# Performance work log

Hardware: AMD Instinct MI355X
Metric: run time of the kernel (lower is better)

The kernel has to match this reference:

```python
import jax, jax.numpy as jnp
import numpy as np
from jax import lax

B, H, W, M, D, HEADS = 4, 32, 32, 16, 128, 4
N = H * W * M
EPS = 1e-5  # torch LayerNorm default


def layer_norm(x, g, b):
    mu = jnp.mean(x, axis=-1, keepdims=True)
    var = jnp.var(x, axis=-1, keepdims=True)
    return (x - mu) * lax.rsqrt(var + EPS) * g + b


def setup_inputs() -> dict:
    key = jax.random.key(0)
    ks = jax.random.split(key, 8)
    s = 0.02  # weight init scale
    return {
        "x1": jax.random.normal(ks[0], (B, N, D), jnp.float32),
        "x2": jax.random.normal(ks[1], (B, N, D), jnp.float32),
        "ln1_g": jnp.ones((D,), jnp.float32),
        "ln1_b": jnp.zeros((D,), jnp.float32),
        "rep_w": jax.random.normal(ks[2], (2 * D, D), jnp.float32) * s,
        "rep_b": jnp.zeros((2 * D,), jnp.float32),
        "aln_g": jnp.ones((2 * D,), jnp.float32),
        "aln_b": jnp.zeros((2 * D,), jnp.float32),
        "ln2_g": jnp.ones((2 * D,), jnp.float32),
        "ln2_b": jnp.zeros((2 * D,), jnp.float32),
        "fc1_w": jax.random.normal(ks[3], (2 * D, 4 * D), jnp.float32) * s,
        "fc1_b": jnp.zeros((4 * D,), jnp.float32),
        "dw_w": jax.random.normal(ks[4], (4 * D, 1, 3, 3, 3), jnp.float32) * s,
        "dw_b": jnp.zeros((4 * D,), jnp.float32),
        "mln_g": jnp.ones((4 * D,), jnp.float32),
        "mln_b": jnp.zeros((4 * D,), jnp.float32),
        "fc2_w": jax.random.normal(ks[5], (4 * D, 2 * D), jnp.float32) * s,
        "fc2_b": jnp.zeros((2 * D,), jnp.float32),
    }


def reference(x1, x2, ln1_g, ln1_b, rep_w, rep_b, aln_g, aln_b, ln2_g, ln2_b,
              fc1_w, fc1_b, dw_w, dw_b, mln_g, mln_b, fc2_w, fc2_b):
    hk = D // HEADS  # head key channels (== head value channels here)

    # shared norm1 applied to both streams
    n1 = layer_norm(x1, ln1_g, ln1_b)
    n2 = layer_norm(x2, ln1_g, ln1_b)

    # linear (softmax-KV) cross attention: K,Q from n2, V from n1
    kq = jnp.transpose(n2, (0, 2, 1)).reshape(B, HEADS, hk, N)
    v = jnp.transpose(n1, (0, 2, 1)).reshape(B, HEADS, hk, N)
    key = jax.nn.softmax(kq, axis=3)    # softmax over tokens N
    query = jax.nn.softmax(kq, axis=2)  # softmax over head channels
    # context: [B,h,hk,hv]; attended: [B,h,hv,N]
    context = jnp.einsum('bhkn,bhvn->bhkv', key, v)
    att = jnp.einsum('bhkv,bhkn->bhvn', context, query)
    agg = att.reshape(B, D, H, W, M)

    # 1x1x1 Conv3d reprojection D -> 2D, then LayerNorm over channels
    rep = jnp.einsum('ed,bdhwm->behwm', rep_w, agg) + rep_b[None, :, None, None, None]
    rep = jnp.transpose(rep.reshape(B, 2 * D, N), (0, 2, 1))
    attn_out = layer_norm(rep, aln_g, aln_b)

    tx = jnp.concatenate([x1, x2], axis=2) + attn_out  # [B,N,2D]

    # MixFFN_skip on norm2(tx)
    y = layer_norm(tx, ln2_g, ln2_b)
    h1 = y @ fc1_w + fc1_b  # [B,N,4D]
    xv = jnp.transpose(h1, (0, 2, 1)).reshape(B, 4 * D, H, W, M)
    dw = lax.conv_general_dilated(
        xv, dw_w, window_strides=(1, 1, 1), padding='SAME',
        dimension_numbers=('NCDHW', 'OIDHW', 'NCDHW'),
        feature_group_count=4 * D) + dw_b[None, :, None, None, None]
    dw = jnp.transpose(dw.reshape(B, 4 * D, N), (0, 2, 1))
    ax = jax.nn.gelu(layer_norm(dw + h1, mln_g, mln_b), approximate=False)
    out = ax @ fc2_w + fc2_b  # [B,N,2D]

    return tx + out
```

## Files before the change

kernel.cpp:

```cpp
#include <hip/hip_runtime.h>
#include <hip/hip_bf16.h>
#include <math.h>

namespace {

typedef __hip_bfloat16 bf16;
typedef __attribute__((ext_vector_type(8))) short bf16x8;
typedef __attribute__((ext_vector_type(4))) float f32x4;

constexpr int B = 4;
constexpr int N = 16384;
constexpr int D = 128;
constexpr int D2 = 256;
constexpr int D4 = 512;
constexpr int HEADS = 4;
constexpr float EPS = 1e-5f;
constexpr long long BN = (long long)B * N;

__device__ __forceinline__ float tof(bf16 x) { return __bfloat162float(x); }
__device__ __forceinline__ bf16 tob(float x) { return __float2bfloat16(x); }
__device__ __forceinline__ float bflo(unsigned u) { union { unsigned i; float f; } c; c.i = u << 16; return c.f; }
__device__ __forceinline__ float bfhi(unsigned u) { union { unsigned i; float f; } c; c.i = u & 0xffff0000u; return c.f; }
__device__ __forceinline__ unsigned short us(float x) {
  union { bf16 h; unsigned short u; } c; c.h = tob(x); return c.u;
}

__device__ __forceinline__ float ldx(const void* p, long long i, int fl) {
  return fl ? ((const float*)p)[i] : tof(((const bf16*)p)[i]);
}
__device__ __forceinline__ void stx(void* p, long long i, int fl, float v) {
  if (fl) ((float*)p)[i] = v; else ((bf16*)p)[i] = tob(v);
}

constexpr size_t OFF_FLAG = 0;
constexpr size_t OFF_KST  = 1024;
constexpr size_t OFF_CTX  = 2048;
constexpr size_t OFF_REPT = 18432;
constexpr size_t OFF_DWW  = 51200;
constexpr size_t OFF_VEC  = 65024;
constexpr size_t OFF_W1S  = 68864;
constexpr size_t OFF_W2S  = 150784;
constexpr size_t OFF_ST1  = 224512;
constexpr size_t OFF_ST2  = 355584;
constexpr size_t OFF_ST3  = 486656;
constexpr size_t OFF_H1   = 617728;

constexpr int CCH = 128;
constexpr size_t OFF_PARTC = OFF_H1;
constexpr size_t OFF_PARTK = OFF_H1 + 2162688;
constexpr size_t OFF_MREP = OFF_H1;

constexpr int V_LN1G = 0, V_LN1B = 128, V_REPB = 256, V_ALNG = 512, V_ALNB = 768,
              V_LN2G = 1024, V_LN2B = 1280, V_FC1B = 1536, V_DWB = 2048,
              V_MLNG = 2560, V_MLNB = 3072, V_FC2B = 3584;

__global__ void k_detect(const unsigned* __restrict__ g1raw, int* __restrict__ flag) {
  if (threadIdx.x == 0 && blockIdx.x == 0)
    *flag = (g1raw[0] == 0x3F800000u) ? 1 : 0;
}

constexpr int CVT_TOTAL = 32768 + 13824 + 3840 + 163840 + 147456;
__global__ __launch_bounds__(256) void k_cvt(const void* rep_w, const void* fc1_w,
                                             const void* fc2_w, const void* dw_w,
                                             const void* ln1_g, const void* ln1_b,
                                             const void* rep_b, const void* aln_g,
                                             const void* aln_b, const void* ln2_g,
                                             const void* ln2_b, const void* fc1_b,
                                             const void* dw_b, const void* mln_g,
                                             const void* mln_b, const void* fc2_b,
                                             float* __restrict__ ws,
                                             const int* __restrict__ flag) {
  int i = blockIdx.x * 256 + threadIdx.x;
  if (i >= CVT_TOTAL) return;
  int fl = *flag;
  if (i < 32768) {
    int e = i >> 7, d = i & 127;
    ws[OFF_REPT + d * D2 + e] = ldx(rep_w, i, fl);
  } else if (i < 46592) {
    int j = i - 32768; ws[OFF_DWW + j] = ldx(dw_w, j, fl);
  } else if (i < 50432) {
    int j = i - 46592;
    const void* src; int off;
    if      (j < 128)  { src = ln1_g; off = j - V_LN1G; }
    else if (j < 256)  { src = ln1_b; off = j - V_LN1B; }
    else if (j < 512)  { src = rep_b; off = j - V_REPB; }
    else if (j < 768)  { src = aln_g; off = j - V_ALNG; }
    else if (j < 1024) { src = aln_b; off = j - V_ALNB; }
    else if (j < 1280) { src = ln2_g; off = j - V_LN2G; }
    else if (j < 1536) { src = ln2_b; off = j - V_LN2B; }
    else if (j < 2048) { src = fc1_b; off = j - V_FC1B; }
    else if (j < 2560) { src = dw_b;  off = j - V_DWB; }
    else if (j < 3072) { src = mln_g; off = j - V_MLNG; }
    else if (j < 3584) { src = mln_b; off = j - V_MLNB; }
    else               { src = fc2_b; off = j - V_FC2B; }
    ws[OFF_VEC + j] = ldx(src, off, fl);
  } else if (i < 214272) {
    int j = i - 50432;
    int kc = j / 20480, rem = j % 20480;
    int n = rem / 40, kk = rem % 40;
    float v = (kk < 32) ? ldx(fc1_w, (kc * 32 + kk) * 512 + n, fl) : 0.f;
    ((unsigned short*)(ws + OFF_W1S))[j] = us(v);
  } else {
    int j = i - 214272;
    int kc = j / 18432, rem = j % 18432;
    int n = rem / 72, kk = rem % 72;
    float v = (kk < 64) ? ldx(fc2_w, (kc * 64 + kk) * 256 + n, fl) : 0.f;
    ((unsigned short*)(ws + OFF_W2S))[j] = us(v);
  }
}

__global__ __launch_bounds__(256) void k_rowstats(const void* __restrict__ x1,
                                                  const void* __restrict__ x2,
                                                  float2* __restrict__ st1,
                                                  float2* __restrict__ st2,
                                                  const int* __restrict__ flag) {
  int fl = *flag;
  int wid = threadIdx.x >> 6;
  int lane = threadIdx.x & 63;
  long long row = (long long)blockIdx.x * 4 + wid;
  const void* src;
  float2* dst;
  long long r;
  if (row < BN) { src = x1; dst = st1; r = row; }
  else          { src = x2; dst = st2; r = row - BN; }
  float a = ldx(src, r * D + lane, fl);
  float b = ldx(src, r * D + lane + 64, fl);
  float s = a + b, ss = a * a + b * b;
  for (int off = 32; off; off >>= 1) {
    s  += __shfl_xor(s, off, 64);
    ss += __shfl_xor(ss, off, 64);
  }
  if (lane == 0) {
    float mu = s * (1.0f / D);
    float var = fmaxf(ss * (1.0f / D) - mu * mu, 0.f);
    dst[r] = make_float2(mu, rsqrtf(var + EPS));
  }
}

__global__ __launch_bounds__(256) void k_kstats_part(const void* __restrict__ x2,
                                                     const float2* __restrict__ st2,
                                                     const float* __restrict__ vec,
                                                     float2* __restrict__ part,
                                                     const int* __restrict__ flag) {
  __shared__ float2 st[256];
  __shared__ float sm[128], ssum[128];
  int fl = *flag;
  int t = threadIdx.x;
  int bc = blockIdx.x;
  int b = bc >> 6;
  int chunk = bc & 63;
  long long tokbase = (long long)b * N + chunk * 256;
  st[t] = st2[tokbase + t];
  __syncthreads();
  int g = t >> 7, c = t & 127;
  float gc = vec[V_LN1G + c], bcv = vec[V_LN1B + c];
  float m = -INFINITY, s = 0.f;
  for (int i = 0; i < 128; i++) {
    int nl = g * 128 + i;
    float2 a2 = st[nl];
    float x = (ldx(x2, (tokbase + nl) * D + c, fl) - a2.x) * a2.y * gc + bcv;
    if (x > m) { s = s * expf(m - x) + 1.f; m = x; }
    else       { s += expf(x - m); }
  }
  if (g == 1) { sm[c] = m; ssum[c] = s; }
  __syncthreads();
  if (g == 0) {
    float m2 = sm[c], s2 = ssum[c];
    float M = fmaxf(m, m2);
    float S = s * expf(m - M) + s2 * expf(m2 - M);
    part[bc * 128 + c] = make_float2(M, S);
  }
}

__global__ __launch_bounds__(256) void k_kstats_fin(const float2* __restrict__ part,
                                                    float* __restrict__ kst) {
  int id = blockIdx.x * 256 + threadIdx.x;
  int b = id >> 7, c = id & 127;
  float m = -INFINITY, s = 0.f;
  for (int ch = 0; ch < 64; ch++) {
    float2 p = part[(b * 64 + ch) * 128 + c];
    float M = fmaxf(m, p.x);
    s = s * expf(m - M) + p.y * expf(p.x - M);
    m = M;
  }
  kst[id * 2] = m;
  kst[id * 2 + 1] = s;
}

__global__ __launch_bounds__(256) void k_ctx_part(const void* __restrict__ x1,
                                                  const void* __restrict__ x2,
                                                  const float2* __restrict__ st1,
                                                  const float2* __restrict__ st2,
                                                  const float* __restrict__ vec,
                                                  const float* __restrict__ kst,
                                                  float* __restrict__ part,
                                                  const int* __restrict__ flag) {
  __shared__ float es[32][128];
  __shared__ float vs[32][128];
  __shared__ float gch[128], bch[128], km[128], kz[128];
  __shared__ float mu2s[32], rs2s[32], rs1s[32], rms[32];
  int fl = *flag;
  int t = threadIdx.x;
  int bc = blockIdx.x;
  int b = bc / CCH, chunk = bc % CCH;
  if (t < 128) {
    gch[t] = vec[V_LN1G + t];
    bch[t] = vec[V_LN1B + t];
    km[t] = kst[(b * 128 + t) * 2];
    kz[t] = 1.f / kst[(b * 128 + t) * 2 + 1];
  }
  int h = t >> 6, lane = t & 63;
  int kg = lane >> 3, vg = lane & 7;
  float acc[4][4];
#pragma unroll
  for (int i = 0; i < 4; i++)
#pragma unroll
    for (int j = 0; j < 4; j++) acc[i][j] = 0.f;
  float sq[4] = {0.f, 0.f, 0.f, 0.f};
  long long tokbase = (long long)b * N + chunk * 128;

  for (int sub = 0; sub < 4; sub++) {
    __syncthreads();
    if (t < 32) {
      float2 a1 = st1[tokbase + sub * 32 + t];
      float2 a2 = st2[tokbase + sub * 32 + t];
      mu2s[t] = a2.x; rs2s[t] = a2.y; rs1s[t] = a1.y; rms[t] = a1.y * a1.x;
    }
    __syncthreads();
    if (fl) {
      for (int i = t; i < 2048; i += 256) {
        int r = i >> 6, cp = i & 63;
        long long off = (tokbase + sub * 32 + r) * D + cp * 2;
        float2 u2 = *(const float2*)((const float*)x2 + off);
        float2 u1 = *(const float2*)((const float*)x1 + off);
        int c0 = cp * 2, c1 = c0 + 1;
        es[r][c0] = expf((u2.x - mu2s[r]) * rs2s[r] * gch[c0] + bch[c0] - km[c0]) * kz[c0];
        es[r][c1] = expf((u2.y - mu2s[r]) * rs2s[r] * gch[c1] + bch[c1] - km[c1]) * kz[c1];
        vs[r][c0] = rs1s[r] * u1.x;
        vs[r][c1] = rs1s[r] * u1.y;
      }
    } else {
      for (int i = t; i < 2048; i += 256) {
        int r = i >> 6, cp = i & 63;
        long long off = (tokbase + sub * 32 + r) * D + cp * 2;
        unsigned u2 = *(const unsigned*)((const bf16*)x2 + off);
        unsigned u1 = *(const unsigned*)((const bf16*)x1 + off);
        int c0 = cp * 2, c1 = c0 + 1;
        es[r][c0] = expf((bflo(u2) - mu2s[r]) * rs2s[r] * gch[c0] + bch[c0] - km[c0]) * kz[c0];
        es[r][c1] = expf((bfhi(u2) - mu2s[r]) * rs2s[r] * gch[c1] + bch[c1] - km[c1]) * kz[c1];
        vs[r][c0] = rs1s[r] * bflo(u1);
        vs[r][c1] = rs1s[r] * bfhi(u1);
      }
    }
    __syncthreads();
#pragma unroll 4
    for (int r = 0; r < 32; r++) {
      float4 ev = *(const float4*)&es[r][h * 32 + kg * 4];
      float4 vv = *(const float4*)&vs[r][h * 32 + vg * 4];
      acc[0][0] += ev.x * vv.x; acc[0][1] += ev.x * vv.y; acc[0][2] += ev.x * vv.z; acc[0][3] += ev.x * vv.w;
      acc[1][0] += ev.y * vv.x; acc[1][1] += ev.y * vv.y; acc[1][2] += ev.y * vv.z; acc[1][3] += ev.y * vv.w;
      acc[2][0] += ev.z * vv.x; acc[2][1] += ev.z * vv.y; acc[2][2] += ev.z * vv.z; acc[2][3] += ev.z * vv.w;
      acc[3][0] += ev.w * vv.x; acc[3][1] += ev.w * vv.y; acc[3][2] += ev.w * vv.z; acc[3][3] += ev.w * vv.w;
      if (vg == 0) {
        float rm = rms[r];
        sq[0] += ev.x * rm; sq[1] += ev.y * rm; sq[2] += ev.z * rm; sq[3] += ev.w * rm;
      }
    }
  }
  float* pb = part + (long long)bc * 4224;
#pragma unroll
  for (int i = 0; i < 4; i++)
#pragma unroll
    for (int j = 0; j < 4; j++)
      pb[h * 1024 + (kg * 4 + i) * 32 + vg * 4 + j] = acc[i][j];
  if (vg == 0) {
#pragma unroll
    for (int i = 0; i < 4; i++)
      pb[4096 + h * 32 + kg * 4 + i] = sq[i];
  }
}

__global__ __launch_bounds__(256) void k_ctx_fin(const float* __restrict__ part,
                                                 const float* __restrict__ vec,
                                                 float* __restrict__ ctx) {
  int id = blockIdx.x * 256 + threadIdx.x;
  int b = id >> 12;
  int hkv = id & 4095;
  int h = hkv >> 10;
  int k = (hkv >> 5) & 31;
  int v = hkv & 31;
  float A = 0.f, SQ = 0.f;
  const float* p = part + (long long)b * CCH * 4224;
  for (int ch = 0; ch < CCH; ch++) {
    A  += p[ch * 4224 + hkv];
    SQ += p[ch * 4224 + 4096 + h * 32 + k];
  }
  ctx[id] = vec[V_LN1G + h * 32 + v] * (A - SQ) + vec[V_LN1B + h * 32 + v];
}

__global__ __launch_bounds__(256) void k_fold(const float* __restrict__ ctx,
                                              const float* __restrict__ repT,
                                              unsigned short* __restrict__ mrep) {
  __shared__ float cs[32][33];
  __shared__ float rs[32][257];
  int t = threadIdx.x;
  int b = blockIdx.x >> 2, h = blockIdx.x & 3;
  const float* cb = ctx + (b * 4 + h) * 1024;
  for (int i = t; i < 1024; i += 256) cs[i >> 5][i & 31] = cb[i];
  for (int v = 0; v < 32; v++) rs[v][t] = repT[(h * 32 + v) * D2 + t];
  __syncthreads();
  float rv[32];
#pragma unroll
  for (int v = 0; v < 32; v++) rv[v] = rs[v][t];
  unsigned short* outp = mrep + ((long long)(b * 4 + h) * 256 + t) * 40;
  for (int k = 0; k < 32; k++) {
    float a = 0.f;
#pragma unroll
    for (int v = 0; v < 32; v++) a += cs[k][v] * rv[v];
    outp[k] = us(a);
  }
#pragma unroll
  for (int k = 32; k < 40; k++) outp[k] = 0;
}

constexpr int TTA = 32;
__global__ __launch_bounds__(256, 4) void k_attn(const void* __restrict__ x1,
                                                 const void* __restrict__ x2,
                                                 const float2* __restrict__ st2,
                                                 const float* __restrict__ vec,
                                                 const unsigned short* __restrict__ mrep,
                                                 void* __restrict__ out,
                                                 float2* __restrict__ st3,
                                                 const int* __restrict__ flag) {
  __shared__ __align__(16) unsigned short qa[32][136];
  __shared__ __align__(16) unsigned short bt[256 * 40];
  __shared__ float gs[128], bs[128];
  __shared__ float pst[2][32][2];
  int fl = *flag;
  int t = threadIdx.x;
  int blk = blockIdx.x;
  int b = blk / (N / TTA);
  long long n0 = (long long)(blk % (N / TTA)) * TTA;
  long long tok0 = (long long)b * N + n0;

  if (t < 128) { gs[t] = vec[V_LN1G + t]; bs[t] = vec[V_LN1B + t]; }

  int r = t >> 3;
  int hc = t & 7;
  float2 a2 = st2[tok0 + r];
  float xv[16];
  long long xbase = (tok0 + r) * D + hc * 16;
  if (fl) {
    const float4* p = (const float4*)((const float*)x2 + xbase);
#pragma unroll
    for (int q = 0; q < 4; q++) {
      float4 u = p[q];
      xv[q * 4 + 0] = u.x; xv[q * 4 + 1] = u.y;
      xv[q * 4 + 2] = u.z; xv[q * 4 + 3] = u.w;
    }
  } else {
#pragma unroll
    for (int i = 0; i < 16; i++) xv[i] = tof(((const bf16*)x2)[xbase + i]);
  }
  __syncthreads();
#pragma unroll
  for (int i = 0; i < 16; i++) {
    int c = hc * 16 + i;
    xv[i] = (xv[i] - a2.x) * a2.y * gs[c] + bs[c];
  }
  float m = xv[0];
#pragma unroll
  for (int i = 1; i < 16; i++) m = fmaxf(m, xv[i]);
  m = fmaxf(m, __shfl_xor(m, 1));
  float s = 0.f;
#pragma unroll
  for (int i = 0; i < 16; i++) { xv[i] = expf(xv[i] - m); s += xv[i]; }
  s += __shfl_xor(s, 1);
  float z = 1.f / s;
#pragma unroll
  for (int i = 0; i < 16; i++) qa[r][hc * 16 + i] = us(xv[i] * z);

  int w = t >> 6, lane = t & 63;
  int m0 = (w & 1) * 16, nh = w >> 1;
  int qm = lane & 15, quad = lane >> 4;
  f32x4 acc[8];
#pragma unroll
  for (int i = 0; i < 8; i++) acc[i] = (f32x4){0.f, 0.f, 0.f, 0.f};
  const uint4* mv = (const uint4*)(mrep + (long long)b * 40960);
  for (int kc = 0; kc < 4; kc++) {
    __syncthreads();
    {
      const uint4* src = mv + kc * 1280;
      uint4* dst = (uint4*)bt;
#pragma unroll
      for (int j = 0; j < 5; j++) dst[t + j * 256] = src[t + j * 256];
    }
    __syncthreads();
    bf16x8 a = *(const bf16x8*)&qa[m0 + qm][kc * 32 + quad * 8];
#pragma unroll
    for (int nt = 0; nt < 8; nt++) {
      bf16x8 bv = *(const bf16x8*)&bt[(nh * 128 + nt * 16 + qm) * 40 + quad * 8];
      acc[nt] = __builtin_amdgcn_mfma_f32_16x16x32_bf16(a, bv, acc[nt], 0, 0, 0);
    }
  }

#pragma unroll
  for (int nt = 0; nt < 8; nt++) {
    float bias = vec[V_REPB + nh * 128 + nt * 16 + qm];
#pragma unroll
    for (int reg = 0; reg < 4; reg++) acc[nt][reg] += bias;
  }

  float s4[4], q4[4];
#pragma unroll
  for (int reg = 0; reg < 4; reg++) {
    float sS = 0.f, sQ = 0.f;
#pragma unroll
    for (int nt = 0; nt < 8; nt++) { float v = acc[nt][reg]; sS += v; sQ += v * v; }
#pragma unroll
    for (int off = 8; off; off >>= 1) {
      sS += __shfl_xor(sS, off, 64);
      sQ += __shfl_xor(sQ, off, 64);
    }
    s4[reg] = sS; q4[reg] = sQ;
  }
  if (qm == 0) {
#pragma unroll
    for (int reg = 0; reg < 4; reg++) {
      int row = m0 + quad * 4 + reg;
      pst[nh][row][0] = s4[reg];
      pst[nh][row][1] = q4[reg];
    }
  }
  __syncthreads();
  float mu4[4], rs4[4];
#pragma unroll
  for (int reg = 0; reg < 4; reg++) {
    int row = m0 + quad * 4 + reg;
    float S = s4[reg] + pst[1 - nh][row][0];
    float Q = q4[reg] + pst[1 - nh][row][1];
    float mu = S * (1.0f / D2);
    float var = fmaxf(Q * (1.0f / D2) - mu * mu, 0.f);
    mu4[reg] = mu; rs4[reg] = rsqrtf(var + EPS);
  }

  const void* xsrc = (nh == 0) ? x1 : x2;
  float s2[4] = {0.f, 0.f, 0.f, 0.f}, q2[4] = {0.f, 0.f, 0.f, 0.f};
#pragma unroll
  for (int nt = 0; nt < 8; nt++) {
    int e = nh * 128 + nt * 16 + qm;
    int col = nt * 16 + qm;
    float ag = vec[V_ALNG + e], ab = vec[V_ALNB + e];
#pragma unroll
    for (int reg = 0; reg < 4; reg++) {
      int row = m0 + quad * 4 + reg;
      long long tok = tok0 + row;
      float val = (acc[nt][reg] - mu4[reg]) * rs4[reg] * ag + ab;
      float base = ldx(xsrc, tok * D + col, fl);
      float txv = val + base;
      stx(out, tok * D2 + e, fl, txv);
      s2[reg] += txv; q2[reg] += txv * txv;
    }
  }
#pragma unroll
  for (int reg = 0; reg < 4; reg++) {
#pragma unroll
    for (int off = 8; off; off >>= 1) {
      s2[reg] += __shfl_xor(s2[reg], off, 64);
      q2[reg] += __shfl_xor(q2[reg], off, 64);
    }
  }
  __syncthreads();
  if (qm == 0) {
#pragma unroll
    for (int reg = 0; reg < 4; reg++) {
      int row = m0 + quad * 4 + reg;
      pst[nh][row][0] = s2[reg];
      pst[nh][row][1] = q2[reg];
    }
  }
  __syncthreads();
  if (nh == 0 && qm == 0) {
#pragma unroll
    for (int reg = 0; reg < 4; reg++) {
      int row = m0 + quad * 4 + reg;
      float S = s2[reg] + pst[1][row][0];
      float Q = q2[reg] + pst[1][row][1];
      float mu = S * (1.0f / D2);
      float var = fmaxf(Q * (1.0f / D2) - mu * mu, 0.f);
      st3[tok0 + row] = make_float2(mu, rsqrtf(var + EPS));
    }
  }
}

__global__ __launch_bounds__(256) void k_fc1m(const void* __restrict__ tx,
                                              long long txbase,
                                              const float2* __restrict__ st3b,
                                              const float* __restrict__ vec,
                                              const unsigned short* __restrict__ w1s,
                                              bf16* __restrict__ h1,
                                              const int* __restrict__ flag) {
  __shared__ __align__(16) unsigned short at[32][264];
  __shared__ __align__(16) unsigned short bt[512 * 40];
  __shared__ float2 sst[32];
  int fl = *flag;
  int t = threadIdx.x;
  int tok0 = blockIdx.x * 32;
  if (t < 32) sst[t] = st3b[tok0 + t];
  __syncthreads();
  for (int i = t; i < 32 * 256; i += 256) {
    int r = i >> 8, c = i & 255;
    float x = ldx(tx, txbase + (long long)(tok0 + r) * D2 + c, fl);
    float2 s = sst[r];
    at[r][c] = us((x - s.x) * s.y * vec[V_LN2G + c] + vec[V_LN2B + c]);
  }
  int w = t >> 6, lane = t & 63;
  int m0 = (w & 1) * 16, nh = w >> 1;
  int qm = lane & 15, quad = lane >> 4;
  f32x4 acc[16];
#pragma unroll
  for (int i = 0; i < 16; i++) acc[i] = (f32x4){0.f, 0.f, 0.f, 0.f};
  const uint4* w1v = (const uint4*)w1s;
  for (int kc = 0; kc < 8; kc++) {
    __syncthreads();
    {
      const uint4* src = w1v + kc * 2560;
      uint4* dst = (uint4*)bt;
#pragma unroll
      for (int j = 0; j < 10; j++) dst[t + j * 256] = src[t + j * 256];
    }
    __syncthreads();
    bf16x8 a = *(const bf16x8*)&at[m0 + qm][kc * 32 + quad * 8];
#pragma unroll
    for (int nt = 0; nt < 16; nt++) {
      bf16x8 b = *(const bf16x8*)&bt[(nh * 256 + nt * 16 + qm) * 40 + quad * 8];
      acc[nt] = __builtin_amdgcn_mfma_f32_16x16x32_bf16(a, b, acc[nt], 0, 0, 0);
    }
  }
#pragma unroll
  for (int nt = 0; nt < 16; nt++) {
    int n = nh * 256 + nt * 16 + qm;
    float bias = vec[V_FC1B + n];
#pragma unroll
    for (int reg = 0; reg < 4; reg++) {
      int row = m0 + quad * 4 + reg;
      h1[(long long)(tok0 + row) * D4 + n] = tob(acc[nt][reg] + bias);
    }
  }
}

__global__ __launch_bounds__(256) void k_dwfc2m(const bf16* __restrict__ h1,
                                                const float* __restrict__ dww,
                                                const float* __restrict__ vec,
                                                const unsigned short* __restrict__ w2s,
                                                void* __restrict__ out,
                                                long long outbase,
                                                const int* __restrict__ flag) {
  __shared__ __align__(16) unsigned short at[16][520];
  __shared__ __align__(16) unsigned short bt[256 * 72];
  __shared__ float redS[4][16], redSS[4][16];
  __shared__ float stat[16][2];
  int fl = *flag;
  int t = threadIdx.x;
  int hh0 = blockIdx.x >> 5, ww0 = blockIdx.x & 31;
  int tok0 = (hh0 << 9) + (ww0 << 4);
  int c0 = t, c1 = t + 256;
  float acc0[16], acc1[16];
  float db0 = vec[V_DWB + c0], db1 = vec[V_DWB + c1];
#pragma unroll
  for (int m = 0; m < 16; m++) { acc0[m] = db0; acc1[m] = db1; }
  for (int dh = -1; dh <= 1; dh++) {
    int hh = hh0 + dh;
    if ((unsigned)hh >= 32u) continue;
    for (int dw2 = -1; dw2 <= 1; dw2++) {
      int ww = ww0 + dw2;
      if ((unsigned)ww >= 32u) continue;
      int nb = (hh << 9) + (ww << 4);
      float va0[18], va1[18];
      va0[0] = 0.f; va0[17] = 0.f; va1[0] = 0.f; va1[17] = 0.f;
#pragma unroll
      for (int j = 0; j < 16; j++) {
        const bf16* p = h1 + (long long)(nb + j) * D4;
        va0[j + 1] = tof(p[c0]);
        va1[j + 1] = tof(p[c1]);
      }
      int jb = (dh + 1) * 9 + (dw2 + 1) * 3;
      float w00 = dww[c0 * 27 + jb], w01 = dww[c0 * 27 + jb + 1], w02 = dww[c0 * 27 + jb + 2];
      float w10 = dww[c1 * 27 + jb], w11 = dww[c1 * 27 + jb + 1], w12 = dww[c1 * 27 + jb + 2];
#pragma unroll
      for (int m = 0; m < 16; m++) {
        acc0[m] += w00 * va0[m] + w01 * va0[m + 1] + w02 * va0[m + 2];
        acc1[m] += w10 * va1[m] + w11 * va1[m + 1] + w12 * va1[m + 2];
      }
    }
  }
  int wid = t >> 6, lane = t & 63;
#pragma unroll
  for (int m = 0; m < 16; m++) {
    const bf16* hp = h1 + (long long)(tok0 + m) * D4;
    acc0[m] += tof(hp[c0]);
    acc1[m] += tof(hp[c1]);
    float s = acc0[m] + acc1[m];
    float ss = acc0[m] * acc0[m] + acc1[m] * acc1[m];
    for (int off = 32; off; off >>= 1) {
      s  += __shfl_xor(s, off, 64);
      ss += __shfl_xor(ss, off, 64);
    }
    if (lane == 0) { redS[wid][m] = s; redSS[wid][m] = ss; }
  }
  __syncthreads();
  if (t < 16) {
    float S  = redS[0][t] + redS[1][t] + redS[2][t] + redS[3][t];
    float SS = redSS[0][t] + redSS[1][t] + redSS[2][t] + redSS[3][t];
    float mu = S * (1.0f / D4);
    float var = fmaxf(SS * (1.0f / D4) - mu * mu, 0.f);
    stat[t][0] = mu;
    stat[t][1] = rsqrtf(var + EPS);
  }
  __syncthreads();
  float g0 = vec[V_MLNG + c0], g1 = vec[V_MLNG + c1];
  float bb0 = vec[V_MLNB + c0], bb1 = vec[V_MLNB + c1];
#pragma unroll
  for (int m = 0; m < 16; m++) {
    float mu = stat[m][0], rs = stat[m][1];
    float y0 = (acc0[m] - mu) * rs * g0 + bb0;
    float y1 = (acc1[m] - mu) * rs * g1 + bb1;
    y0 = 0.5f * y0 * (1.f + erff(y0 * 0.70710678118654752f));
    y1 = 0.5f * y1 * (1.f + erff(y1 * 0.70710678118654752f));
    at[m][c0] = us(y0);
    at[m][c1] = us(y1);
  }
  int qm = lane & 15, quad = lane >> 4;
  int nbase = wid * 64;
  f32x4 acc[4];
#pragma unroll
  for (int i = 0; i < 4; i++) acc[i] = (f32x4){0.f, 0.f, 0.f, 0.f};
  const uint4* w2v = (const uint4*)w2s;
  for (int kc = 0; kc < 8; kc++) {
    __syncthreads();
    {
      const uint4* src = w2v + kc * 2304;
      uint4* dst = (uint4*)bt;
#pragma unroll
      for (int j = 0; j < 9; j++) dst[t + j * 256] = src[t + j * 256];
    }
    __syncthreads();
#pragma unroll
    for (int ks = 0; ks < 2; ks++) {
      bf16x8 a = *(const bf16x8*)&at[qm][kc * 64 + ks * 32 + quad * 8];
#pragma unroll
      for (int nt = 0; nt < 4; nt++) {
        bf16x8 b = *(const bf16x8*)&bt[(nbase + nt * 16 + qm) * 72 + ks * 32 + quad * 8];
        acc[nt] = __builtin_amdgcn_mfma_f32_16x16x32_bf16(a, b, acc[nt], 0, 0, 0);
      }
    }
  }
#pragma unroll
  for (int nt = 0; nt < 4; nt++) {
    int n = nbase + nt * 16 + qm;
    float bias = vec[V_FC2B + n];
#pragma unroll
    for (int reg = 0; reg < 4; reg++) {
      int row = quad * 4 + reg;
      long long o = outbase + (long long)(tok0 + row) * D2 + n;
      stx(out, o, fl, ldx(out, o, fl) + acc[nt][reg] + bias);
    }
  }
}

}

extern "C" void kernel_launch(void* const* d_in, const int* in_sizes, int n_in,
                              void* d_out, int out_size, void* d_ws, size_t ws_size,
                              hipStream_t stream) {
  float* ws = (float*)d_ws;
  int*    flag  = (int*)(ws + OFF_FLAG);
  float*  kst   = ws + OFF_KST;
  float*  ctx   = ws + OFF_CTX;
  float*  repT  = ws + OFF_REPT;
  float*  dww   = ws + OFF_DWW;
  float*  vec   = ws + OFF_VEC;
  unsigned short* w1s = (unsigned short*)(ws + OFF_W1S);
  unsigned short* w2s = (unsigned short*)(ws + OFF_W2S);
  float2* st1   = (float2*)(ws + OFF_ST1);
  float2* st2   = (float2*)(ws + OFF_ST2);
  float2* st3   = (float2*)(ws + OFF_ST3);
  float*  partc = ws + OFF_PARTC;
  float2* partk = (float2*)(ws + OFF_PARTK);
  unsigned short* mrep = (unsigned short*)(ws + OFF_MREP);
  bf16*   h1    = (bf16*)(ws + OFF_H1);

  hipLaunchKernelGGL(k_detect, dim3(1), dim3(64), 0, stream,
                     (const unsigned*)d_in[2], flag);
  hipLaunchKernelGGL(k_cvt, dim3(CVT_TOTAL / 256), dim3(256), 0, stream,
                     d_in[4], d_in[10], d_in[16], d_in[12],
                     d_in[2], d_in[3], d_in[5], d_in[6], d_in[7], d_in[8],
                     d_in[9], d_in[11], d_in[13], d_in[14], d_in[15], d_in[17],
                     ws, flag);
  hipLaunchKernelGGL(k_rowstats, dim3((unsigned)(2 * BN / 4)), dim3(256), 0, stream,
                     d_in[0], d_in[1], st1, st2, flag);
  hipLaunchKernelGGL(k_kstats_part, dim3(B * 64), dim3(256), 0, stream,
                     d_in[1], st2, vec, partk, flag);
  hipLaunchKernelGGL(k_kstats_fin, dim3(2), dim3(256), 0, stream, partk, kst);
  hipLaunchKernelGGL(k_ctx_part, dim3(B * CCH), dim3(256), 0, stream,
                     d_in[0], d_in[1], st1, st2, vec, kst, partc, flag);
  hipLaunchKernelGGL(k_ctx_fin, dim3(64), dim3(256), 0, stream, partc, vec, ctx);
  hipLaunchKernelGGL(k_fold, dim3(B * HEADS), dim3(256), 0, stream, ctx, repT, mrep);
  hipLaunchKernelGGL(k_attn, dim3((unsigned)(BN / TTA)), dim3(256), 0, stream,
                     d_in[0], d_in[1], st2, vec, mrep, d_out, st3, flag);
  for (int b = 0; b < B; b++) {
    long long base = (long long)b * N * D2;
    hipLaunchKernelGGL(k_fc1m, dim3(N / 32), dim3(256), 0, stream,
                       d_out, base, st3 + (long long)b * N, vec, w1s, h1, flag);
    hipLaunchKernelGGL(k_dwfc2m, dim3(N / 16), dim3(256), 0, stream,
                       h1, dww, vec, w2s, d_out, base, flag);
  }
}
```

Before: 667.8 us.

## Read GEMM weight fragments directly from global memory instead of staging in LDS

In the attention, fc1 and dwconv+fc2 kernels, the per-k-chunk cooperative copy of the weight tile into shared memory is removed, along with its two barriers per iteration. MFMA B fragments are now loaded straight from global memory, which relies on L2/L1 caching since the weights are shared by every block. This cuts LDS use and is meant to raise occupancy (launch bounds now request 4 blocks per SM), at the cost of more, less coalesced global loads. The depthwise conv also switches to interleaved channel pairs so each thread loads packed 32-bit bf16 pairs.

```diff
diff --git a/kernel.cpp b/kernel.cpp
--- a/kernel.cpp
+++ b/kernel.cpp
@@ -333,7 +333,6 @@
                                                  float2* __restrict__ st3,
                                                  const int* __restrict__ flag) {
   __shared__ __align__(16) unsigned short qa[32][136];
-  __shared__ __align__(16) unsigned short bt[256 * 40];
   __shared__ float gs[128], bs[128];
   __shared__ float pst[2][32][2];
   int fl = *flag;
@@ -379,6 +378,7 @@
   float z = 1.f / s;
 #pragma unroll
   for (int i = 0; i < 16; i++) qa[r][hc * 16 + i] = us(xv[i] * z);
+  __syncthreads();
 
   int w = t >> 6, lane = t & 63;
   int m0 = (w & 1) * 16, nh = w >> 1;
@@ -386,20 +386,14 @@
   f32x4 acc[8];
 #pragma unroll
   for (int i = 0; i < 8; i++) acc[i] = (f32x4){0.f, 0.f, 0.f, 0.f};
-  const uint4* mv = (const uint4*)(mrep + (long long)b * 40960);
+  const unsigned short* mb = mrep + (long long)b * 40960;
+#pragma unroll
   for (int kc = 0; kc < 4; kc++) {
-    __syncthreads();
-    {
-      const uint4* src = mv + kc * 1280;
-      uint4* dst = (uint4*)bt;
-#pragma unroll
-      for (int j = 0; j < 5; j++) dst[t + j * 256] = src[t + j * 256];
-    }
-    __syncthreads();
     bf16x8 a = *(const bf16x8*)&qa[m0 + qm][kc * 32 + quad * 8];
 #pragma unroll
     for (int nt = 0; nt < 8; nt++) {
-      bf16x8 bv = *(const bf16x8*)&bt[(nh * 128 + nt * 16 + qm) * 40 + quad * 8];
+      int e = nh * 128 + nt * 16 + qm;
+      bf16x8 bv = *(const bf16x8*)(mb + kc * 10240 + e * 40 + quad * 8);
       acc[nt] = __builtin_amdgcn_mfma_f32_16x16x32_bf16(a, bv, acc[nt], 0, 0, 0);
     }
   }
@@ -493,15 +487,14 @@
   }
 }
 
-__global__ __launch_bounds__(256) void k_fc1m(const void* __restrict__ tx,
-                                              long long txbase,
-                                              const float2* __restrict__ st3b,
-                                              const float* __restrict__ vec,
-                                              const unsigned short* __restrict__ w1s,
-                                              bf16* __restrict__ h1,
-                                              const int* __restrict__ flag) {
+__global__ __launch_bounds__(256, 4) void k_fc1m(const void* __restrict__ tx,
+                                                 long long txbase,
+                                                 const float2* __restrict__ st3b,
+                                                 const float* __restrict__ vec,
+                                                 const unsigned short* __restrict__ w1s,
+                                                 bf16* __restrict__ h1,
+                                                 const int* __restrict__ flag) {
   __shared__ __align__(16) unsigned short at[32][264];
-  __shared__ __align__(16) unsigned short bt[512 * 40];
   __shared__ float2 sst[32];
   int fl = *flag;
   int t = threadIdx.x;
@@ -514,26 +507,21 @@
     float2 s = sst[r];
     at[r][c] = us((x - s.x) * s.y * vec[V_LN2G + c] + vec[V_LN2B + c]);
   }
+  __syncthreads();
   int w = t >> 6, lane = t & 63;
   int m0 = (w & 1) * 16, nh = w >> 1;
   int qm = lane & 15, quad = lane >> 4;
   f32x4 acc[16];
 #pragma unroll
   for (int i = 0; i < 16; i++) acc[i] = (f32x4){0.f, 0.f, 0.f, 0.f};
-  const uint4* w1v = (const uint4*)w1s;
+#pragma unroll
   for (int kc = 0; kc < 8; kc++) {
-    __syncthreads();
-    {
-      const uint4* src = w1v + kc * 2560;
-      uint4* dst = (uint4*)bt;
-#pragma unroll
-      for (int j = 0; j < 10; j++) dst[t + j * 256] = src[t + j * 256];
-    }
-    __syncthreads();
     bf16x8 a = *(const bf16x8*)&at[m0 + qm][kc * 32 + quad * 8];
+    const unsigned short* wp = w1s + kc * 20480 + quad * 8;
 #pragma unroll
     for (int nt = 0; nt < 16; nt++) {
-      bf16x8 b = *(const bf16x8*)&bt[(nh * 256 + nt * 16 + qm) * 40 + quad * 8];
+      int n = nh * 256 + nt * 16 + qm;
+      bf16x8 b = *(const bf16x8*)(wp + n * 40);
       acc[nt] = __builtin_amdgcn_mfma_f32_16x16x32_bf16(a, b, acc[nt], 0, 0, 0);
     }
   }
@@ -549,22 +537,21 @@
   }
 }
 
-__global__ __launch_bounds__(256) void k_dwfc2m(const bf16* __restrict__ h1,
-                                                const float* __restrict__ dww,
-                                                const float* __restrict__ vec,
-                                                const unsigned short* __restrict__ w2s,
-                                                void* __restrict__ out,
-                                                long long outbase,
-                                                const int* __restrict__ flag) {
+__global__ __launch_bounds__(256, 4) void k_dwfc2m(const bf16* __restrict__ h1,
+                                                   const float* __restrict__ dww,
+                                                   const float* __restrict__ vec,
+                                                   const unsigned short* __restrict__ w2s,
+                                                   void* __restrict__ out,
+                                                   long long outbase,
+                                                   const int* __restrict__ flag) {
   __shared__ __align__(16) unsigned short at[16][520];
-  __shared__ __align__(16) unsigned short bt[256 * 72];
   __shared__ float redS[4][16], redSS[4][16];
   __shared__ float stat[16][2];
   int fl = *flag;
   int t = threadIdx.x;
   int hh0 = blockIdx.x >> 5, ww0 = blockIdx.x & 31;
   int tok0 = (hh0 << 9) + (ww0 << 4);
-  int c0 = t, c1 = t + 256;
+  int c0 = 2 * t, c1 = 2 * t + 1;
   float acc0[16], acc1[16];
   float db0 = vec[V_DWB + c0], db1 = vec[V_DWB + c1];
 #pragma unroll
@@ -578,11 +565,12 @@
       int nb = (hh << 9) + (ww << 4);
       float va0[18], va1[18];
       va0[0] = 0.f; va0[17] = 0.f; va1[0] = 0.f; va1[17] = 0.f;
+      const unsigned short* p = (const unsigned short*)h1 + ((long long)nb * D4 + c0);
 #pragma unroll
       for (int j = 0; j < 16; j++) {
-        const bf16* p = h1 + (long long)(nb + j) * D4;
-        va0[j + 1] = tof(p[c0]);
-        va1[j + 1] = tof(p[c1]);
+        unsigned u = *(const unsigned*)(p + (size_t)j * D4);
+        va0[j + 1] = bflo(u);
+        va1[j + 1] = bfhi(u);
       }
       int jb = (dh + 1) * 9 + (dw2 + 1) * 3;
       float w00 = dww[c0 * 27 + jb], w01 = dww[c0 * 27 + jb + 1], w02 = dww[c0 * 27 + jb + 2];
@@ -595,18 +583,21 @@
     }
   }
   int wid = t >> 6, lane = t & 63;
-#pragma unroll
-  for (int m = 0; m < 16; m++) {
-    const bf16* hp = h1 + (long long)(tok0 + m) * D4;
-    acc0[m] += tof(hp[c0]);
-    acc1[m] += tof(hp[c1]);
-    float s = acc0[m] + acc1[m];
-    float ss = acc0[m] * acc0[m] + acc1[m] * acc1[m];
-    for (int off = 32; off; off >>= 1) {
-      s  += __shfl_xor(s, off, 64);
-      ss += __shfl_xor(ss, off, 64);
-    }
-    if (lane == 0) { redS[wid][m] = s; redSS[wid][m] = ss; }
+  {
+    const unsigned short* hp = (const unsigned short*)h1 + ((long long)tok0 * D4 + c0);
+#pragma unroll
+    for (int m = 0; m < 16; m++) {
+      unsigned u = *(const unsigned*)(hp + (size_t)m * D4);
+      acc0[m] += bflo(u);
+      acc1[m] += bfhi(u);
+      float s = acc0[m] + acc1[m];
+      float ss = acc0[m] * acc0[m] + acc1[m] * acc1[m];
+      for (int off = 32; off; off >>= 1) {
+        s  += __shfl_xor(s, off, 64);
+        ss += __shfl_xor(ss, off, 64);
+      }
+      if (lane == 0) { redS[wid][m] = s; redSS[wid][m] = ss; }
+    }
   }
   __syncthreads();
   if (t < 16) {
@@ -627,30 +618,24 @@
     float y1 = (acc1[m] - mu) * rs * g1 + bb1;
     y0 = 0.5f * y0 * (1.f + erff(y0 * 0.70710678118654752f));
     y1 = 0.5f * y1 * (1.f + erff(y1 * 0.70710678118654752f));
-    at[m][c0] = us(y0);
-    at[m][c1] = us(y1);
-  }
+    *(unsigned*)&at[m][c0] = (unsigned)us(y0) | ((unsigned)us(y1) << 16);
+  }
+  __syncthreads();
   int qm = lane & 15, quad = lane >> 4;
   int nbase = wid * 64;
   f32x4 acc[4];
 #pragma unroll
   for (int i = 0; i < 4; i++) acc[i] = (f32x4){0.f, 0.f, 0.f, 0.f};
-  const uint4* w2v = (const uint4*)w2s;
+#pragma unroll
   for (int kc = 0; kc < 8; kc++) {
-    __syncthreads();
-    {
-      const uint4* src = w2v + kc * 2304;
-      uint4* dst = (uint4*)bt;
-#pragma unroll
-      for (int j = 0; j < 9; j++) dst[t + j * 256] = src[t + j * 256];
-    }
-    __syncthreads();
 #pragma unroll
     for (int ks = 0; ks < 2; ks++) {
       bf16x8 a = *(const bf16x8*)&at[qm][kc * 64 + ks * 32 + quad * 8];
+      const unsigned short* wp = w2s + kc * 18432 + ks * 32 + quad * 8;
 #pragma unroll
       for (int nt = 0; nt < 4; nt++) {
-        bf16x8 b = *(const bf16x8*)&bt[(nbase + nt * 16 + qm) * 72 + ks * 32 + quad * 8];
+        int n = nbase + nt * 16 + qm;
+        bf16x8 b = *(const bf16x8*)(wp + n * 72);
         acc[nt] = __builtin_amdgcn_mfma_f32_16x16x32_bf16(a, b, acc[nt], 0, 0, 0);
       }
     }
```

Measured after the change: 671.6 us. About the same (+0.6%).
